# Kernel tuning notes

Hardware: AMD Instinct MI355X
Metric: run time of the kernel (lower is better)

## Reference

```python
import jax, jax.numpy as jnp
import numpy as np

B, L, D_MODEL = 2, 2048, 1024
EXPAND, D_STATE, D_CONV = 2, 16, 4
D_INNER = EXPAND * D_MODEL
DT_RANK = D_MODEL // 16  # mamba default: ceil(d_model/16)


def setup_inputs() -> dict:
    key = jax.random.key(0)
    ks = jax.random.split(key, 8)
    s = 0.02
    return {
        "x": jax.random.normal(ks[0], (B, L, D_MODEL), jnp.float32),
        "in_proj_w": jax.random.normal(ks[1], (2 * D_INNER, D_MODEL), jnp.float32) * s,
        "conv_w": jax.random.normal(ks[2], (D_INNER, D_CONV), jnp.float32) * s,
        "conv_b": jnp.zeros((D_INNER,), jnp.float32),
        "x_proj_w": jax.random.normal(ks[3], (DT_RANK + 2 * D_STATE, D_INNER), jnp.float32) * s,
        "dt_proj_w": jax.random.normal(ks[4], (D_INNER, DT_RANK), jnp.float32) * s,
        "dt_proj_b": jnp.full((D_INNER,), -4.6, jnp.float32),  # softplus(-4.6) ~ 0.01 dt init
        "A_log": jnp.log(jnp.broadcast_to(jnp.arange(1, D_STATE + 1, dtype=jnp.float32), (D_INNER, D_STATE))),
        "D": jnp.ones((D_INNER,), jnp.float32),
        "ssm_out_w": jax.random.normal(ks[5], (D_MODEL, D_INNER), jnp.float32) * s,
        "final_w": jax.random.normal(ks[6], (D_MODEL, D_MODEL), jnp.float32) * s,
        "final_b": jnp.zeros((D_MODEL,), jnp.float32),
    }


def _forward(x, in_proj_w, conv_w, conv_b, x_proj_w, dt_proj_w, dt_proj_b,
             A_log, D, ssm_out_w, final_w, final_b):
    d_inner, d_state = A_log.shape
    dt_rank = dt_proj_w.shape[1]
    d_conv = conv_w.shape[1]

    # in_proj -> split into x-branch and gate z  (B, L, 2*d_inner)
    xz = jnp.einsum('bld,ed->ble', x, in_proj_w)
    xin, z = jnp.split(xz, 2, axis=-1)

    # causal depthwise conv1d over time, then SiLU
    xc = jax.lax.conv_general_dilated(
        xin.swapaxes(1, 2),               # (B, d_inner, L)
        conv_w[:, None, :],               # (O=d_inner, I/g=1, W=d_conv)
        window_strides=(1,),
        padding=[(d_conv - 1, 0)],
        dimension_numbers=('NCH', 'OIH', 'NCH'),
        feature_group_count=d_inner,
    )
    xc = jax.nn.silu(xc + conv_b[None, :, None]).swapaxes(1, 2)  # (B, L, d_inner)

    # input-dependent SSM parameters
    x_dbl = jnp.einsum('bld,ed->ble', xc, x_proj_w)              # (B, L, dt_rank+2*d_state)
    dt, Bm, Cm = jnp.split(x_dbl, [dt_rank, dt_rank + d_state], axis=-1)
    delta = jax.nn.softplus(jnp.einsum('blr,dr->bld', dt, dt_proj_w) + dt_proj_b)  # (B,L,d_inner)
    A = -jnp.exp(A_log)                                          # (d_inner, d_state)

    # selective scan: h_t = exp(dt*A) h_{t-1} + dt*B_t*u_t ; y_t = <h_t, C_t>
    def step(h, t):
        delta_t, B_t, C_t, u_t = t                               # (B,Di), (B,N), (B,N), (B,Di)
        h = jnp.exp(delta_t[..., None] * A) * h + (delta_t * u_t)[..., None] * B_t[:, None, :]
        return h, jnp.einsum('bdn,bn->bd', h, C_t)

    h0 = jnp.zeros((x.shape[0], d_inner, d_state), x.dtype)
    xs = (delta.swapaxes(0, 1), Bm.swapaxes(0, 1), Cm.swapaxes(0, 1), xc.swapaxes(0, 1))
    _, ys = jax.lax.scan(step, h0, xs)                           # (L, B, d_inner)

    y = ys.swapaxes(0, 1) + xc * D                               # skip term D*u
    y = y * jax.nn.silu(z)                                       # gating
    out = jnp.einsum('bld,md->blm', y, ssm_out_w)                # Mamba out_proj -> d_model
    # wrapper: Linear(d_model, d_model) then SiLU
    return jax.nn.silu(jnp.einsum('blm,nm->bln', out, final_w) + final_b)


def reference(x, in_proj_w, conv_w, conv_b, x_proj_w, dt_proj_w, dt_proj_b,
              A_log, D, ssm_out_w, final_w, final_b):
    return _forward(x, in_proj_w, conv_w, conv_b, x_proj_w, dt_proj_w, dt_proj_b,
                    A_log, D, ssm_out_w, final_w, final_b)
```

## Files before the change

kernel.cpp:

```cpp
#include <hip/hip_runtime.h>
#include <hip/hip_bf16.h>
#include <math.h>

#define BB 2
#define LL 2048
#define DMODEL 1024
#define DINNER 2048
#define DSTATE 16
#define DCONV 4
#define DTRANK 64
#define MROWS (BB * LL)
#define XPROJ_N (DTRANK + 2 * DSTATE)

#define SEG 64
#define LS (LL / SEG)

#define XKSPLIT 8
#define XKC (DINNER / XKSPLIT)

typedef unsigned short ushort_t;
typedef short s8v __attribute__((ext_vector_type(8)));
typedef float f4v __attribute__((ext_vector_type(4)));

__device__ __forceinline__ float siluf(float x) {
    return x / (1.f + expf(-x));
}
__device__ __forceinline__ float softplusf(float x) {
    return fmaxf(x, 0.f) + log1pf(expf(-fabsf(x)));
}
__device__ __forceinline__ ushort_t f32_to_bf16(float f) {
    unsigned u = __builtin_bit_cast(unsigned, f);
    unsigned r = (u + 0x7FFFu + ((u >> 16) & 1u)) >> 16;
    return (ushort_t)r;
}
__device__ __forceinline__ float bf16_to_f32(ushort_t u) {
    return __builtin_bit_cast(float, ((unsigned)u) << 16);
}

__global__ __launch_bounds__(256) void prep_kernel(
    const float* __restrict__ x, const float* __restrict__ ipw,
    const float* __restrict__ sow, const float* __restrict__ fw,
    const float* __restrict__ xpw, const float* __restrict__ dtw,
    ushort_t* __restrict__ x_bf, ushort_t* __restrict__ ipw_bf,
    ushort_t* __restrict__ sow_bf, ushort_t* __restrict__ fw_bf,
    ushort_t* __restrict__ xpw_bf, ushort_t* __restrict__ dtw_bf,
    float4* __restrict__ xdbl_zero)
{
    const long i = ((long)blockIdx.x * 256 + threadIdx.x) * 4;
    const float* src; ushort_t* dst; long off;
    if      (i < 4194304L)  { src = x;   dst = x_bf;   off = i; }
    else if (i < 8388608L)  { src = ipw; dst = ipw_bf; off = i - 4194304L; }
    else if (i < 10485760L) { src = sow; dst = sow_bf; off = i - 8388608L; }
    else if (i < 11534336L) { src = fw;  dst = fw_bf;  off = i - 10485760L; }
    else if (i < 11730944L) { src = xpw; dst = xpw_bf; off = i - 11534336L; }
    else if (i < 11862016L) { src = dtw; dst = dtw_bf; off = i - 11730944L; }
    else { xdbl_zero[(i - 11862016L) >> 2] = make_float4(0.f, 0.f, 0.f, 0.f); return; }
    const float4 v = *reinterpret_cast<const float4*>(src + off);
    ushort_t o[4] = {f32_to_bf16(v.x), f32_to_bf16(v.y),
                     f32_to_bf16(v.z), f32_to_bf16(v.w)};
    *reinterpret_cast<uint2*>(dst + off) = *reinterpret_cast<uint2*>(o);
}

__global__ __launch_bounds__(256) void cast_dt_kernel(
    const float* __restrict__ xdbl, ushort_t* __restrict__ dtbf)
{
    const int i4 = (blockIdx.x * 256 + threadIdx.x) * 4;
    const int row = i4 >> 6;
    const int col = i4 & 63;
    const float4 v = *reinterpret_cast<const float4*>(&xdbl[(size_t)row * XPROJ_N + col]);
    ushort_t o[4] = {f32_to_bf16(v.x), f32_to_bf16(v.y),
                     f32_to_bf16(v.z), f32_to_bf16(v.w)};
    *reinterpret_cast<uint2*>(dtbf + i4) = *reinterpret_cast<uint2*>(o);
}

#define TM 128
#define TN 128
#define TBK 32

__global__ __launch_bounds__(512) void gemm_bf16_mfma(
    const ushort_t* __restrict__ A, int lda,
    const ushort_t* __restrict__ B, int ldb,
    int K,
    void* __restrict__ C0v, void* __restrict__ C1v, int splitN, int ldc,
    const float* __restrict__ bias, int act, int store_bf16)
{
    __shared__ __align__(16) ushort_t As[TM * TBK];
    __shared__ __align__(16) ushort_t Bs[TN * TBK];

    const int tid  = threadIdx.x;
    const int lane = tid & 63;
    const int w    = tid >> 6;
    const int wm   = w & 1;
    const int wn   = w >> 1;
    const int m0   = blockIdx.y * TM;
    const int n0   = blockIdx.x * TN;

    const int srow = lane >> 2;
    const int scol = (lane & 3) * 8;

    f4v acc[4][2] = {};

    for (int k0 = 0; k0 < K; k0 += TBK) {
        {
            const ushort_t* ga = A + (size_t)(m0 + w * 16 + srow) * lda + k0 + scol;
            __builtin_amdgcn_global_load_lds(
                (const __attribute__((address_space(1))) unsigned int*)ga,
                (__attribute__((address_space(3))) unsigned int*)(As + w * 512),
                16, 0, 0);
        }
        {
            const ushort_t* gb = B + (size_t)(n0 + w * 16 + srow) * ldb + k0 + scol;
            __builtin_amdgcn_global_load_lds(
                (const __attribute__((address_space(1))) unsigned int*)gb,
                (__attribute__((address_space(3))) unsigned int*)(Bs + w * 512),
                16, 0, 0);
        }
        __syncthreads();

        const int fr = lane & 15;
        const int kg = lane >> 4;
        s8v a[4], b[2];
        #pragma unroll
        for (int t = 0; t < 4; ++t)
            a[t] = *reinterpret_cast<const s8v*>(As + (wm * 64 + t * 16 + fr) * TBK + kg * 8);
        #pragma unroll
        for (int t = 0; t < 2; ++t)
            b[t] = *reinterpret_cast<const s8v*>(Bs + (wn * 32 + t * 16 + fr) * TBK + kg * 8);
        #pragma unroll
        for (int i = 0; i < 4; ++i)
            #pragma unroll
            for (int j = 0; j < 2; ++j)
                acc[i][j] = __builtin_amdgcn_mfma_f32_16x16x32_bf16(
                    a[i], b[j], acc[i][j], 0, 0, 0);
        __syncthreads();
    }

    const int rbase = (lane >> 4) * 4;
    const int cbase = lane & 15;
    #pragma unroll
    for (int i = 0; i < 4; ++i) {
        #pragma unroll
        for (int j = 0; j < 2; ++j) {
            const int row = m0 + wm * 64 + i * 16 + rbase;
            const int col = n0 + wn * 32 + j * 16 + cbase;
            void* Cp = C0v;
            int c2 = col;
            if (C1v && col >= splitN) { Cp = C1v; c2 = col - splitN; }
            const float bv = bias ? bias[col] : 0.f;
            #pragma unroll
            for (int r = 0; r < 4; ++r) {
                float v = acc[i][j][r] + bv;
                if (act == 1) v = siluf(v);
                else if (act == 2) v = softplusf(v);
                if (store_bf16)
                    ((ushort_t*)Cp)[(size_t)(row + r) * ldc + c2] = f32_to_bf16(v);
                else
                    ((float*)Cp)[(size_t)(row + r) * ldc + c2] = v;
            }
        }
    }
}

#define UM 64
#define UN 128

__global__ __launch_bounds__(512) void gemm64_bf16_mfma(
    const ushort_t* __restrict__ A, int lda,
    const ushort_t* __restrict__ B, int ldb,
    int K,
    void* __restrict__ C0v, int ldc,
    const float* __restrict__ bias, int act, int store_bf16)
{
    __shared__ __align__(16) ushort_t As[UM * TBK];
    __shared__ __align__(16) ushort_t Bs[UN * TBK];

    const int tid  = threadIdx.x;
    const int lane = tid & 63;
    const int w    = tid >> 6;
    const int wm   = w & 1;
    const int wn   = w >> 1;
    const int m0   = blockIdx.y * UM;
    const int n0   = blockIdx.x * UN;

    const int srow = lane >> 2;
    const int scol = (lane & 3) * 8;

    f4v acc[2][2] = {};

    for (int k0 = 0; k0 < K; k0 += TBK) {
        if (w < 4) {
            const ushort_t* ga = A + (size_t)(m0 + w * 16 + srow) * lda + k0 + scol;
            __builtin_amdgcn_global_load_lds(
                (const __attribute__((address_space(1))) unsigned int*)ga,
                (__attribute__((address_space(3))) unsigned int*)(As + w * 512),
                16, 0, 0);
        }
        {
            const ushort_t* gb = B + (size_t)(n0 + w * 16 + srow) * ldb + k0 + scol;
            __builtin_amdgcn_global_load_lds(
                (const __attribute__((address_space(1))) unsigned int*)gb,
                (__attribute__((address_space(3))) unsigned int*)(Bs + w * 512),
                16, 0, 0);
        }
        __syncthreads();

        const int fr = lane & 15;
        const int kg = lane >> 4;
        s8v a[2], b[2];
        #pragma unroll
        for (int t = 0; t < 2; ++t)
            a[t] = *reinterpret_cast<const s8v*>(As + (wm * 32 + t * 16 + fr) * TBK + kg * 8);
        #pragma unroll
        for (int t = 0; t < 2; ++t)
            b[t] = *reinterpret_cast<const s8v*>(Bs + (wn * 32 + t * 16 + fr) * TBK + kg * 8);
        #pragma unroll
        for (int i = 0; i < 2; ++i)
            #pragma unroll
            for (int j = 0; j < 2; ++j)
                acc[i][j] = __builtin_amdgcn_mfma_f32_16x16x32_bf16(
                    a[i], b[j], acc[i][j], 0, 0, 0);
        __syncthreads();
    }

    const int rbase = (lane >> 4) * 4;
    const int cbase = lane & 15;
    #pragma unroll
    for (int i = 0; i < 2; ++i) {
        #pragma unroll
        for (int j = 0; j < 2; ++j) {
            const int row = m0 + wm * 32 + i * 16 + rbase;
            const int col = n0 + wn * 32 + j * 16 + cbase;
            const float bv = bias ? bias[col] : 0.f;
            #pragma unroll
            for (int r = 0; r < 4; ++r) {
                float v = acc[i][j][r] + bv;
                if (act == 1) v = siluf(v);
                else if (act == 2) v = softplusf(v);
                if (store_bf16)
                    ((ushort_t*)C0v)[(size_t)(row + r) * ldc + col] = f32_to_bf16(v);
                else
                    ((float*)C0v)[(size_t)(row + r) * ldc + col] = v;
            }
        }
    }
}

__global__ __launch_bounds__(256) void xproj_mfma(
    const ushort_t* __restrict__ A, const ushort_t* __restrict__ Bw,
    float* __restrict__ Cout)
{
    __shared__ __align__(16) ushort_t As[64 * 32];
    __shared__ __align__(16) ushort_t Bs[96 * 32];

    const int tid = threadIdx.x;
    const int lane = tid & 63;
    const int w = tid >> 6;
    const int kbase = blockIdx.x * XKC;
    const int m0 = blockIdx.y * 64;

    const int srow = lane >> 2;
    const int scol = (lane & 3) * 8;

    f4v acc[6] = {};

    for (int k0 = kbase; k0 < kbase + XKC; k0 += 32) {
        {
            const ushort_t* ga = A + (size_t)(m0 + w * 16 + srow) * DINNER + k0 + scol;
            __builtin_amdgcn_global_load_lds(
                (const __attribute__((address_space(1))) unsigned int*)ga,
                (__attribute__((address_space(3))) unsigned int*)(As + (w * 16) * 32),
                16, 0, 0);
        }
        {
            const ushort_t* gb = Bw + (size_t)(w * 16 + srow) * DINNER + k0 + scol;
            __builtin_amdgcn_global_load_lds(
                (const __attribute__((address_space(1))) unsigned int*)gb,
                (__attribute__((address_space(3))) unsigned int*)(Bs + (w * 16) * 32),
                16, 0, 0);
        }
        if (w < 2) {
            const ushort_t* gb = Bw + (size_t)((4 + w) * 16 + srow) * DINNER + k0 + scol;
            __builtin_amdgcn_global_load_lds(
                (const __attribute__((address_space(1))) unsigned int*)gb,
                (__attribute__((address_space(3))) unsigned int*)(Bs + ((4 + w) * 16) * 32),
                16, 0, 0);
        }
        __syncthreads();

        const int fr = lane & 15;
        const int kg = lane >> 4;
        const s8v a = *reinterpret_cast<const s8v*>(As + (w * 16 + fr) * 32 + kg * 8);
        #pragma unroll
        for (int j = 0; j < 6; ++j) {
            const s8v b = *reinterpret_cast<const s8v*>(Bs + (j * 16 + fr) * 32 + kg * 8);
            acc[j] = __builtin_amdgcn_mfma_f32_16x16x32_bf16(a, b, acc[j], 0, 0, 0);
        }
        __syncthreads();
    }

    const int rbase = (lane >> 4) * 4;
    const int cb = lane & 15;
    #pragma unroll
    for (int j = 0; j < 6; ++j)
        #pragma unroll
        for (int r = 0; r < 4; ++r)
            atomicAdd(&Cout[(size_t)(m0 + w * 16 + rbase + r) * XPROJ_N + j * 16 + cb],
                      acc[j][r]);
}

__global__ __launch_bounds__(256) void conv_silu_kernel(
    const ushort_t* __restrict__ xin, const float* __restrict__ w,
    const float* __restrict__ b, ushort_t* __restrict__ xcbf)
{
    const int bl = blockIdx.x;
    const int l  = bl & (LL - 1);
    const int c0 = threadIdx.x * 8;

    float acc[8];
    {
        const float4 b0 = *reinterpret_cast<const float4*>(b + c0);
        const float4 b1 = *reinterpret_cast<const float4*>(b + c0 + 4);
        acc[0] = b0.x; acc[1] = b0.y; acc[2] = b0.z; acc[3] = b0.w;
        acc[4] = b1.x; acc[5] = b1.y; acc[6] = b1.z; acc[7] = b1.w;
    }
    float4 wj[8];
    #pragma unroll
    for (int j = 0; j < 8; ++j)
        wj[j] = *reinterpret_cast<const float4*>(w + (c0 + j) * DCONV);

    #pragma unroll
    for (int k = 0; k < DCONV; ++k) {
        const int ll = l - (DCONV - 1) + k;
        if (ll >= 0) {
            const s8v v = *reinterpret_cast<const s8v*>(
                xin + (size_t)(bl - (DCONV - 1) + k) * DINNER + c0);
            #pragma unroll
            for (int j = 0; j < 8; ++j) {
                const float wv = (k == 0) ? wj[j].x : (k == 1) ? wj[j].y
                               : (k == 2) ? wj[j].z : wj[j].w;
                acc[j] = fmaf(bf16_to_f32((ushort_t)v[j]), wv, acc[j]);
            }
        }
    }

    ushort_t o[8];
    #pragma unroll
    for (int j = 0; j < 8; ++j)
        o[j] = f32_to_bf16(siluf(acc[j]));
    *reinterpret_cast<uint4*>(xcbf + (size_t)bl * DINNER + c0) =
        *reinterpret_cast<uint4*>(o);
}

__global__ __launch_bounds__(256) void scan_part1(
    const ushort_t* __restrict__ delta, const float* __restrict__ xdbl,
    const ushort_t* __restrict__ xc, const float* __restrict__ A_log,
    float* __restrict__ hloc, float* __restrict__ sum_dl_out)
{
    const int d = blockIdx.x * 256 + threadIdx.x;
    const int seg = blockIdx.y;
    const int b = blockIdx.z;
    const int t0 = seg * LS;

    float Ad[DSTATE];
    #pragma unroll
    for (int n = 0; n < DSTATE; ++n)
        Ad[n] = -expf(A_log[d * DSTATE + n]);

    float h[DSTATE];
    #pragma unroll
    for (int n = 0; n < DSTATE; ++n) h[n] = 0.f;

    const ushort_t* dp = delta + ((size_t)b * LL) * DINNER + d;
    const ushort_t* up = xc    + ((size_t)b * LL) * DINNER + d;
    const float*    xb = xdbl  + ((size_t)b * LL) * XPROJ_N;

    float sum_dl = 0.f;
    for (int t = t0; t < t0 + LS; ++t) {
        const float dl = bf16_to_f32(dp[(size_t)t * DINNER]);
        const float u  = bf16_to_f32(up[(size_t)t * DINNER]);
        const float4 b0 = *reinterpret_cast<const float4*>(&xb[t * XPROJ_N + DTRANK + 0]);
        const float4 b1 = *reinterpret_cast<const float4*>(&xb[t * XPROJ_N + DTRANK + 4]);
        const float4 b2 = *reinterpret_cast<const float4*>(&xb[t * XPROJ_N + DTRANK + 8]);
        const float4 b3 = *reinterpret_cast<const float4*>(&xb[t * XPROJ_N + DTRANK + 12]);
        const float Bv[DSTATE] = {b0.x, b0.y, b0.z, b0.w, b1.x, b1.y, b1.z, b1.w,
                                  b2.x, b2.y, b2.z, b2.w, b3.x, b3.y, b3.z, b3.w};
        const float dlu = dl * u;
        sum_dl += dl;
        #pragma unroll
        for (int n = 0; n < DSTATE; ++n)
            h[n] = __expf(dl * Ad[n]) * h[n] + dlu * Bv[n];
    }

    const size_t base = (((size_t)b * SEG + seg) * DSTATE) * DINNER + d;
    #pragma unroll
    for (int n = 0; n < DSTATE; ++n)
        hloc[base + (size_t)n * DINNER] = h[n];
    sum_dl_out[((size_t)b * SEG + seg) * DINNER + d] = sum_dl;
}

__global__ __launch_bounds__(256) void scan_combine(
    float* __restrict__ hloc, const float* __restrict__ sum_dl,
    const float* __restrict__ A_log)
{
    const int idx = blockIdx.x * 256 + threadIdx.x;
    const int d = idx % DINNER;
    const int n = (idx / DINNER) % DSTATE;
    const int b = idx / (DINNER * DSTATE);
    if (b >= BB) return;

    const float Ad = -expf(A_log[d * DSTATE + n]);

    const size_t stride = (size_t)DSTATE * DINNER;
    float* __restrict__ hp =
        hloc + (size_t)b * SEG * stride + (size_t)n * DINNER + d;
    const float* __restrict__ sp =
        sum_dl + (size_t)b * SEG * DINNER + d;

    float carry = 0.f;
    #pragma unroll 1
    for (int s8 = 0; s8 < SEG; s8 += 8) {
        float hl[8], dc[8];
        #pragma unroll
        for (int q = 0; q < 8; ++q) {
            hl[q] = hp[(size_t)(s8 + q) * stride];
            dc[q] = sp[(size_t)(s8 + q) * DINNER];
        }
        #pragma unroll
        for (int q = 0; q < 8; ++q)
            dc[q] = __expf(Ad * dc[q]);
        #pragma unroll
        for (int q = 0; q < 8; ++q) {
            hp[(size_t)(s8 + q) * stride] = carry;
            carry = fmaf(dc[q], carry, hl[q]);
        }
    }
}

__global__ __launch_bounds__(256) void scan_part2(
    const ushort_t* __restrict__ delta, const float* __restrict__ xdbl,
    const ushort_t* __restrict__ xc, const ushort_t* __restrict__ z,
    const float* __restrict__ A_log, const float* __restrict__ Dvec,
    const float* __restrict__ hstart, ushort_t* __restrict__ ybf)
{
    const int d = blockIdx.x * 256 + threadIdx.x;
    const int seg = blockIdx.y;
    const int b = blockIdx.z;
    const int t0 = seg * LS;

    float Ad[DSTATE];
    #pragma unroll
    for (int n = 0; n < DSTATE; ++n)
        Ad[n] = -expf(A_log[d * DSTATE + n]);

    float h[DSTATE];
    const size_t hbase = (((size_t)b * SEG + seg) * DSTATE) * DINNER + d;
    #pragma unroll
    for (int n = 0; n < DSTATE; ++n)
        h[n] = hstart[hbase + (size_t)n * DINNER];

    const float Dd = Dvec[d];
    const ushort_t* dp = delta + ((size_t)b * LL) * DINNER + d;
    const ushort_t* up = xc    + ((size_t)b * LL) * DINNER + d;
    const float*    xb = xdbl  + ((size_t)b * LL) * XPROJ_N;
    const ushort_t* zp = z     + ((size_t)b * LL) * DINNER + d;
    ushort_t*       yp = ybf   + ((size_t)b * LL) * DINNER + d;

    for (int t = t0; t < t0 + LS; ++t) {
        const float dl = bf16_to_f32(dp[(size_t)t * DINNER]);
        const float u  = bf16_to_f32(up[(size_t)t * DINNER]);
        const float zv = bf16_to_f32(zp[(size_t)t * DINNER]);
        const float4 b0 = *reinterpret_cast<const float4*>(&xb[t * XPROJ_N + DTRANK + 0]);
        const float4 b1 = *reinterpret_cast<const float4*>(&xb[t * XPROJ_N + DTRANK + 4]);
        const float4 b2 = *reinterpret_cast<const float4*>(&xb[t * XPROJ_N + DTRANK + 8]);
        const float4 b3 = *reinterpret_cast<const float4*>(&xb[t * XPROJ_N + DTRANK + 12]);
        const float4 c0 = *reinterpret_cast<const float4*>(&xb[t * XPROJ_N + DTRANK + DSTATE + 0]);
        const float4 c1 = *reinterpret_cast<const float4*>(&xb[t * XPROJ_N + DTRANK + DSTATE + 4]);
        const float4 c2 = *reinterpret_cast<const float4*>(&xb[t * XPROJ_N + DTRANK + DSTATE + 8]);
        const float4 c3 = *reinterpret_cast<const float4*>(&xb[t * XPROJ_N + DTRANK + DSTATE + 12]);
        const float Bv[DSTATE] = {b0.x, b0.y, b0.z, b0.w, b1.x, b1.y, b1.z, b1.w,
                                  b2.x, b2.y, b2.z, b2.w, b3.x, b3.y, b3.z, b3.w};
        const float Cv[DSTATE] = {c0.x, c0.y, c0.z, c0.w, c1.x, c1.y, c1.z, c1.w,
                                  c2.x, c2.y, c2.z, c2.w, c3.x, c3.y, c3.z, c3.w};
        const float dlu = dl * u;
        float y = 0.f;
        #pragma unroll
        for (int n = 0; n < DSTATE; ++n) {
            h[n] = __expf(dl * Ad[n]) * h[n] + dlu * Bv[n];
            y = fmaf(h[n], Cv[n], y);
        }
        yp[(size_t)t * DINNER] = f32_to_bf16((y + u * Dd) * siluf(zv));
    }
}

extern "C" void kernel_launch(void* const* d_in, const int* in_sizes, int n_in,
                              void* d_out, int out_size, void* d_ws, size_t ws_size,
                              hipStream_t stream) {
    const float* x         = (const float*)d_in[0];
    const float* in_proj_w = (const float*)d_in[1];
    const float* conv_w    = (const float*)d_in[2];
    const float* conv_b    = (const float*)d_in[3];
    const float* x_proj_w  = (const float*)d_in[4];
    const float* dt_proj_w = (const float*)d_in[5];
    const float* dt_proj_b = (const float*)d_in[6];
    const float* A_log     = (const float*)d_in[7];
    const float* Dvec      = (const float*)d_in[8];
    const float* ssm_out_w = (const float*)d_in[9];
    const float* final_w   = (const float*)d_in[10];
    const float* final_b   = (const float*)d_in[11];
    float* out = (float*)d_out;

    const size_t MB = 1024 * 1024;
    char* base = (char*)d_ws;
    ushort_t* xin_bf   = (ushort_t*)(base);
    ushort_t* z_bf     = (ushort_t*)(base + 16 * MB);
    ushort_t* xc_bf    = (ushort_t*)(base + 32 * MB);
    ushort_t* delta_bf = (ushort_t*)(base + 48 * MB);
    float*    xdbl     = (float*)(base + 64 * MB);
    float*    sum_dl   = (float*)(base + 66 * MB);
    ushort_t* x_bf     = (ushort_t*)(base + 78 * MB);
    ushort_t* ipw_bf   = (ushort_t*)(base + 86 * MB);
    ushort_t* sow_bf   = (ushort_t*)(base + 94 * MB);
    ushort_t* fw_bf    = (ushort_t*)(base + 98 * MB);
    ushort_t* xpw_bf   = (ushort_t*)(base + 100 * MB);
    ushort_t* dtw_bf   = (ushort_t*)(base + 100 * MB + 512 * 1024);
    ushort_t* dt_bf    = (ushort_t*)(base + 101 * MB);
    ushort_t* y_bf     = (ushort_t*)(base + 102 * MB);
    ushort_t* outb_bf  = (ushort_t*)(base + 118 * MB);
    float* hloc = (float*)(base);

    prep_kernel<<<11968, 256, 0, stream>>>(
        x, in_proj_w, ssm_out_w, final_w, x_proj_w, dt_proj_w,
        x_bf, ipw_bf, sow_bf, fw_bf, xpw_bf, dtw_bf, (float4*)xdbl);

    gemm_bf16_mfma<<<dim3(2 * DINNER / TN, MROWS / TM), 512, 0, stream>>>(
        x_bf, DMODEL, ipw_bf, DMODEL, DMODEL,
        xin_bf, z_bf, DINNER, DINNER, nullptr, 0, 1);

    conv_silu_kernel<<<MROWS, 256, 0, stream>>>(
        xin_bf, conv_w, conv_b, xc_bf);

    xproj_mfma<<<dim3(XKSPLIT, MROWS / 64), 256, 0, stream>>>(xc_bf, xpw_bf, xdbl);

    cast_dt_kernel<<<(MROWS * DTRANK / 4) / 256, 256, 0, stream>>>(xdbl, dt_bf);
    gemm64_bf16_mfma<<<dim3(DINNER / UN, MROWS / UM), 512, 0, stream>>>(
        dt_bf, DTRANK, dtw_bf, DTRANK, DTRANK,
        delta_bf, DINNER, dt_proj_b, 2, 1);

    scan_part1<<<dim3(DINNER / 256, SEG, BB), 256, 0, stream>>>(
        delta_bf, xdbl, xc_bf, A_log, hloc, sum_dl);
    scan_combine<<<(BB * DSTATE * DINNER) / 256, 256, 0, stream>>>(
        hloc, sum_dl, A_log);
    scan_part2<<<dim3(DINNER / 256, SEG, BB), 256, 0, stream>>>(
        delta_bf, xdbl, xc_bf, z_bf, A_log, Dvec, hloc, y_bf);

    gemm64_bf16_mfma<<<dim3(DMODEL / UN, MROWS / UM), 512, 0, stream>>>(
        y_bf, DINNER, sow_bf, DINNER, DINNER,
        outb_bf, DMODEL, nullptr, 0, 1);

    gemm64_bf16_mfma<<<dim3(DMODEL / UN, MROWS / UM), 512, 0, stream>>>(
        outb_bf, DMODEL, fw_bf, DMODEL, DMODEL,
        out, DMODEL, final_b, 1, 0);
}
```

Baseline: 369.6 us.

## Fuse dt cast into dt_proj GEMM and deepen K tile with swizzled LDS

```diff
diff --git a/kernel.cpp b/kernel.cpp
--- a/kernel.cpp
+++ b/kernel.cpp
@@ -59,18 +59,6 @@
     ushort_t o[4] = {f32_to_bf16(v.x), f32_to_bf16(v.y),
                      f32_to_bf16(v.z), f32_to_bf16(v.w)};
     *reinterpret_cast<uint2*>(dst + off) = *reinterpret_cast<uint2*>(o);
-}
-
-__global__ __launch_bounds__(256) void cast_dt_kernel(
-    const float* __restrict__ xdbl, ushort_t* __restrict__ dtbf)
-{
-    const int i4 = (blockIdx.x * 256 + threadIdx.x) * 4;
-    const int row = i4 >> 6;
-    const int col = i4 & 63;
-    const float4 v = *reinterpret_cast<const float4*>(&xdbl[(size_t)row * XPROJ_N + col]);
-    ushort_t o[4] = {f32_to_bf16(v.x), f32_to_bf16(v.y),
-                     f32_to_bf16(v.z), f32_to_bf16(v.w)};
-    *reinterpret_cast<uint2*>(dtbf + i4) = *reinterpret_cast<uint2*>(o);
 }
 
 #define TM 128
@@ -163,16 +151,18 @@
 
 #define UM 64
 #define UN 128
+#define UBK 64
 
 __global__ __launch_bounds__(512) void gemm64_bf16_mfma(
     const ushort_t* __restrict__ A, int lda,
+    const float* __restrict__ A32, int lda32,
     const ushort_t* __restrict__ B, int ldb,
     int K,
     void* __restrict__ C0v, int ldc,
     const float* __restrict__ bias, int act, int store_bf16)
 {
-    __shared__ __align__(16) ushort_t As[UM * TBK];
-    __shared__ __align__(16) ushort_t Bs[UN * TBK];
+    __shared__ __align__(16) ushort_t As[UM * UBK];
+    __shared__ __align__(16) ushort_t Bs[UN * UBK];
 
     const int tid  = threadIdx.x;
     const int lane = tid & 63;
@@ -182,43 +172,68 @@
     const int m0   = blockIdx.y * UM;
     const int n0   = blockIdx.x * UN;
 
-    const int srow = lane >> 2;
-    const int scol = (lane & 3) * 8;
+    const int sr   = tid >> 3;
+    const int sc   = (tid & 7) * 8;
+    const int scs  = sc ^ ((sr & 7) << 3);
 
     f4v acc[2][2] = {};
 
-    for (int k0 = 0; k0 < K; k0 += TBK) {
-        if (w < 4) {
-            const ushort_t* ga = A + (size_t)(m0 + w * 16 + srow) * lda + k0 + scol;
+    for (int k0 = 0; k0 < K; k0 += UBK) {
+        if (A32) {
+            const float* ga = A32 + (size_t)(m0 + sr) * lda32 + k0 + sc;
+            const float4 v0 = *reinterpret_cast<const float4*>(ga);
+            const float4 v1 = *reinterpret_cast<const float4*>(ga + 4);
+            ushort_t o[8] = {f32_to_bf16(v0.x), f32_to_bf16(v0.y),
+                             f32_to_bf16(v0.z), f32_to_bf16(v0.w),
+                             f32_to_bf16(v1.x), f32_to_bf16(v1.y),
+                             f32_to_bf16(v1.z), f32_to_bf16(v1.w)};
+            *reinterpret_cast<uint4*>(
+                (char*)As + sr * 128 + ((sc * 2) ^ ((sr & 7) << 4)))
+                = *reinterpret_cast<uint4*>(o);
+        } else {
+            const ushort_t* ga = A + (size_t)(m0 + sr) * lda + k0 + scs;
             __builtin_amdgcn_global_load_lds(
                 (const __attribute__((address_space(1))) unsigned int*)ga,
-                (__attribute__((address_space(3))) unsigned int*)(As + w * 512),
+                (__attribute__((address_space(3))) unsigned int*)(As + tid * 8),
                 16, 0, 0);
         }
         {
-            const ushort_t* gb = B + (size_t)(n0 + w * 16 + srow) * ldb + k0 + scol;
+            const ushort_t* gb = B + (size_t)(n0 + sr) * ldb + k0 + scs;
             __builtin_amdgcn_global_load_lds(
                 (const __attribute__((address_space(1))) unsigned int*)gb,
-                (__attribute__((address_space(3))) unsigned int*)(Bs + w * 512),
+                (__attribute__((address_space(3))) unsigned int*)(Bs + tid * 8),
+                16, 0, 0);
+            const ushort_t* gb2 = B + (size_t)(n0 + 64 + sr) * ldb + k0 + scs;
+            __builtin_amdgcn_global_load_lds(
+                (const __attribute__((address_space(1))) unsigned int*)gb2,
+                (__attribute__((address_space(3))) unsigned int*)(Bs + 4096 + tid * 8),
                 16, 0, 0);
         }
         __syncthreads();
 
-        const int fr = lane & 15;
-        const int kg = lane >> 4;
-        s8v a[2], b[2];
-        #pragma unroll
-        for (int t = 0; t < 2; ++t)
-            a[t] = *reinterpret_cast<const s8v*>(As + (wm * 32 + t * 16 + fr) * TBK + kg * 8);
-        #pragma unroll
-        for (int t = 0; t < 2; ++t)
-            b[t] = *reinterpret_cast<const s8v*>(Bs + (wn * 32 + t * 16 + fr) * TBK + kg * 8);
+        const int fr  = lane & 15;
+        const int kg  = lane >> 4;
+        const int swr = (fr & 7) << 4;
+        s8v a[2][2], b[2][2];
+        #pragma unroll
+        for (int i = 0; i < 2; ++i)
+            #pragma unroll
+            for (int ks = 0; ks < 2; ++ks) {
+                a[i][ks] = *reinterpret_cast<const s8v*>(
+                    (const char*)As + (wm * 32 + i * 16 + fr) * 128
+                                    + ((ks * 64 + kg * 16) ^ swr));
+                b[i][ks] = *reinterpret_cast<const s8v*>(
+                    (const char*)Bs + (wn * 32 + i * 16 + fr) * 128
+                                    + ((ks * 64 + kg * 16) ^ swr));
+            }
         #pragma unroll
         for (int i = 0; i < 2; ++i)
             #pragma unroll
             for (int j = 0; j < 2; ++j)
-                acc[i][j] = __builtin_amdgcn_mfma_f32_16x16x32_bf16(
-                    a[i], b[j], acc[i][j], 0, 0, 0);
+                #pragma unroll
+                for (int ks = 0; ks < 2; ++ks)
+                    acc[i][j] = __builtin_amdgcn_mfma_f32_16x16x32_bf16(
+                        a[i][ks], b[j][ks], acc[i][j], 0, 0, 0);
         __syncthreads();
     }
 
@@ -523,7 +538,6 @@
     ushort_t* fw_bf    = (ushort_t*)(base + 98 * MB);
     ushort_t* xpw_bf   = (ushort_t*)(base + 100 * MB);
     ushort_t* dtw_bf   = (ushort_t*)(base + 100 * MB + 512 * 1024);
-    ushort_t* dt_bf    = (ushort_t*)(base + 101 * MB);
     ushort_t* y_bf     = (ushort_t*)(base + 102 * MB);
     ushort_t* outb_bf  = (ushort_t*)(base + 118 * MB);
     float* hloc = (float*)(base);
@@ -541,9 +555,8 @@
 
     xproj_mfma<<<dim3(XKSPLIT, MROWS / 64), 256, 0, stream>>>(xc_bf, xpw_bf, xdbl);
 
-    cast_dt_kernel<<<(MROWS * DTRANK / 4) / 256, 256, 0, stream>>>(xdbl, dt_bf);
     gemm64_bf16_mfma<<<dim3(DINNER / UN, MROWS / UM), 512, 0, stream>>>(
-        dt_bf, DTRANK, dtw_bf, DTRANK, DTRANK,
+        nullptr, 0, xdbl, XPROJ_N, dtw_bf, DTRANK, DTRANK,
         delta_bf, DINNER, dt_proj_b, 2, 1);
 
     scan_part1<<<dim3(DINNER / 256, SEG, BB), 256, 0, stream>>>(
@@ -554,10 +567,10 @@
         delta_bf, xdbl, xc_bf, z_bf, A_log, Dvec, hloc, y_bf);
 
     gemm64_bf16_mfma<<<dim3(DMODEL / UN, MROWS / UM), 512, 0, stream>>>(
-        y_bf, DINNER, sow_bf, DINNER, DINNER,
+        y_bf, DINNER, nullptr, 0, sow_bf, DINNER, DINNER,
         outb_bf, DMODEL, nullptr, 0, 1);
 
     gemm64_bf16_mfma<<<dim3(DMODEL / UN, MROWS / UM), 512, 0, stream>>>(
-        outb_bf, DMODEL, fw_bf, DMODEL, DMODEL,
+        outb_bf, DMODEL, nullptr, 0, fw_bf, DMODEL, DMODEL,
         out, DMODEL, final_b, 1, 0);
 }
```

After: 361.0 us. 1.02x faster.
